# Optimization experiments

Measured on AMD Instinct MI355X. Metric: run time of the kernel, lower is better.

## Reference

```python
import jax, jax.numpy as jnp
import numpy as np

B = 4096          # batch
IN = 4096         # in_features
OUT = 4096        # out_features
MASK_DENSITY = 0.1

def setup_inputs() -> dict:
    key = jax.random.key(0)
    k1, k2, k3, k4, k5 = jax.random.split(key, 5)
    x = jax.random.normal(k1, (B, IN), dtype=jnp.float32)
    # truncated-normal-ish init, std 0.1 (plain normal scaled is fine for a numeric baseline)
    weight = jax.random.normal(k2, (OUT, IN), dtype=jnp.float32) * 0.1
    bound = 1.0 / np.sqrt(IN)
    bias = jax.random.uniform(k3, (OUT,), dtype=jnp.float32, minval=-bound, maxval=bound)
    mask = jax.random.bernoulli(k4, MASK_DENSITY, (OUT, IN))  # bool, fixed sparsity pattern
    residual_connection = jax.random.randint(k5, (OUT,), 0, IN, dtype=jnp.int32)
    return {"x": x, "weight": weight, "bias": bias, "mask": mask,
            "residual_connection": residual_connection}

def reference(x, weight, bias, mask, residual_connection):
    # out = relu(x @ (mask * W)^T + b) + x[:, residual_connection]
    w_masked = jnp.where(mask, weight, 0.0)              # [OUT, IN]
    out = x @ w_masked.T + bias                          # [B, OUT]
    out = jax.nn.relu(out)
    out = jnp.take(x, residual_connection, axis=1) + out # gathered residual add
    return out
```

## Files before the change

kernel.cpp:

```cpp
#include <hip/hip_runtime.h>
#include <hip/hip_bf16.h>
#include <stdint.h>

#define B_ROWS 4096
#define IN_F   4096
#define OUT_F  4096

#define BM 256
#define BN 256
#define BK 64
#define NKT (IN_F / BK)

typedef float  f32x4  __attribute__((ext_vector_type(4)));
typedef short  bf16x8 __attribute__((ext_vector_type(8)));
typedef unsigned short u16x4 __attribute__((ext_vector_type(4)));

#define AS1 __attribute__((address_space(1)))
#define AS3 __attribute__((address_space(3)))

template<int N> struct IC { static constexpr int v = N; };

__device__ __forceinline__ uint16_t f2bf_rne(float f) {
    uint32_t u = __float_as_uint(f);
    uint32_t r = u + 0x7fffu + ((u >> 16) & 1u);
    return (uint16_t)(r >> 16);
}
__device__ __forceinline__ float bf2f(uint16_t h) {
    return __uint_as_float(((uint32_t)h) << 16);
}

__global__ __launch_bounds__(256) void prep_kernel(
    const float* __restrict__ x, uint16_t* __restrict__ xb, uint16_t* __restrict__ xbT,
    const float* __restrict__ w, const void* __restrict__ mraw, uint16_t* __restrict__ wb)
{
    __shared__ float t[64][65];
    __shared__ int flag_s;
    const int tid = threadIdx.x;
    const int blk = blockIdx.x;

    if (blk < 4096) {
        const int r0 = (blk >> 6) * 64;
        const int c0 = (blk & 63) * 64;
        const int lr = tid >> 4;
        const int lc4 = (tid & 15) * 4;

#pragma unroll
        for (int p = 0; p < 4; ++p) {
            const int row = p * 16 + lr;
            float4 v = *(const float4*)(x + (size_t)(r0 + row) * IN_F + c0 + lc4);
            ushort4 o;
            o.x = f2bf_rne(v.x); o.y = f2bf_rne(v.y);
            o.z = f2bf_rne(v.z); o.w = f2bf_rne(v.w);
            *(ushort4*)(xb + (size_t)(r0 + row) * IN_F + c0 + lc4) = o;
            t[row][lc4 + 0] = v.x; t[row][lc4 + 1] = v.y;
            t[row][lc4 + 2] = v.z; t[row][lc4 + 3] = v.w;
        }
        __syncthreads();
#pragma unroll
        for (int p = 0; p < 4; ++p) {
            const int c = p * 16 + lr;
            ushort4 o;
            o.x = f2bf_rne(t[lc4 + 0][c]);
            o.y = f2bf_rne(t[lc4 + 1][c]);
            o.z = f2bf_rne(t[lc4 + 2][c]);
            o.w = f2bf_rne(t[lc4 + 3][c]);
            *(ushort4*)(xbT + (size_t)(c0 + c) * B_ROWS + r0 + lc4) = o;
        }
    } else {
        uint32_t mword = ((const uint32_t*)mraw)[tid];
        unsigned long long bal = __ballot((mword & 0xFFFFFF00u) != 0);
        if (tid == 0) flag_s = 0;
        __syncthreads();
        if (bal != 0ull && (tid & 63) == 0) flag_s = 1;
        __syncthreads();
        const int flag = flag_s;

        const int i = ((blk - 4096) * 256 + tid) * 4;
        float4 v = *(const float4*)(w + i);
        int m0, m1, m2, m3;
        if (flag) {
            uchar4 mm = *(const uchar4*)((const uint8_t*)mraw + i);
            m0 = mm.x; m1 = mm.y; m2 = mm.z; m3 = mm.w;
        } else {
            int4 mm = *(const int4*)((const int*)mraw + i);
            m0 = mm.x; m1 = mm.y; m2 = mm.z; m3 = mm.w;
        }
        ushort4 o;
        o.x = m0 ? f2bf_rne(v.x) : (uint16_t)0;
        o.y = m1 ? f2bf_rne(v.y) : (uint16_t)0;
        o.z = m2 ? f2bf_rne(v.z) : (uint16_t)0;
        o.w = m3 ? f2bf_rne(v.w) : (uint16_t)0;
        *(ushort4*)(wb + i) = o;
    }
}

__device__ __forceinline__ bf16x8 ds_read128(uint32_t off) {
    bf16x8 r;
    asm volatile("ds_read_b128 %0, %1" : "=v"(r) : "v"(off));
    return r;
}
#define LDSOFF(p) ((uint32_t)(uintptr_t)(AS3 void*)(p))

__global__ __launch_bounds__(512, 2) void gemm_kernel(
    const uint16_t* __restrict__ xb, const uint16_t* __restrict__ wb,
    const uint16_t* __restrict__ xbT, const float* __restrict__ bias,
    const int* __restrict__ rc, float* __restrict__ out)
{
    __shared__ alignas(16) uint16_t Abuf[2][2][128 * BK];
    __shared__ alignas(16) uint16_t Bbuf[2][2][128 * BK];
    __shared__ float bias_s[BN];
    __shared__ int   rc_s[BN];

    const int tid = threadIdx.x;

    const int bid = blockIdx.x;
    const int wg  = (bid & 7) * 32 + (bid >> 3);
    const int row0 = (wg >> 4) * BM;
    const int col0 = (wg & 15) * BN;

    const int wave = tid >> 6, lane = tid & 63;
    const int wm = wave >> 2;
    const int wn = wave & 3;
    const int bh = wn >> 1;
    const int quad = lane >> 4, l16 = lane & 15;
    const int swr = (l16 & 7) << 3;
    const int e0  = (quad << 3) ^ swr;
    const uint32_t kd = (uint32_t)(((e0 ^ 32) - e0) * 2);

    const uint32_t aOff0 = LDSOFF(&Abuf[0][wm][0]) + (uint32_t)((l16 * BK + e0) * 2);
    const uint32_t aOff1 = LDSOFF(&Abuf[1][wm][0]) + (uint32_t)((l16 * BK + e0) * 2);
    const uint32_t bOff0 = LDSOFF(&Bbuf[0][bh][0]) + (uint32_t)((((wn & 1) * 64 + l16) * BK + e0) * 2);
    const uint32_t bOff1 = LDSOFF(&Bbuf[1][bh][0]) + (uint32_t)((((wn & 1) * 64 + l16) * BK + e0) * 2);

    const int srow = tid >> 3;
    const int ssw  = ((tid & 7) ^ (srow & 7)) << 3;
    const uint16_t* pA0 = xb + (size_t)(row0 + srow) * IN_F + ssw;
    const uint16_t* pB0 = wb + (size_t)(col0 + srow) * IN_F + ssw;
    const uint16_t* pA1 = pA0 + (size_t)128 * IN_F;
    const uint16_t* pB1 = pB0 + (size_t)128 * IN_F;

    auto stage = [&](const uint16_t* src, uint16_t* ldsdst, size_t ko) {
        __builtin_amdgcn_global_load_lds((const AS1 void*)(src + ko),
                                         (AS3 void*)(ldsdst + tid * 8), 16, 0, 0);
        __builtin_amdgcn_global_load_lds((const AS1 void*)(src + ko + (size_t)64 * IN_F),
                                         (AS3 void*)(ldsdst + tid * 8 + 4096), 16, 0, 0);
    };

    if (tid < BN) {
        __builtin_amdgcn_global_load_lds((const AS1 void*)(bias + col0 + tid),
                                         (AS3 void*)(bias_s + tid), 4, 0, 0);
        __builtin_amdgcn_global_load_lds((const AS1 void*)(rc + col0 + tid),
                                         (AS3 void*)(rc_s + tid), 4, 0, 0);
    }

    f32x4 acc[8][4];
#pragma unroll
    for (int mi = 0; mi < 8; ++mi)
#pragma unroll
        for (int ni = 0; ni < 4; ++ni)
            acc[mi][ni] = (f32x4){0.f, 0.f, 0.f, 0.f};

    stage(pA0, &Abuf[0][0][0], 0);
    stage(pA1, &Abuf[0][1][0], 0);
    stage(pB0, &Bbuf[0][0][0], 0);
    stage(pB1, &Bbuf[0][1][0], 0);

#define LGKM0() do { asm volatile("s_waitcnt lgkmcnt(0)" ::: "memory"); \
                     __builtin_amdgcn_sched_barrier(0); } while (0)

    auto tile = [&](auto curc, int t) {
        constexpr int CUR = decltype(curc)::v;
        constexpr int NXT = CUR ^ 1;
        const uint32_t aB = CUR ? aOff1 : aOff0;
        const uint32_t bB = CUR ? bOff1 : bOff0;
        const size_t koff = (size_t)(t + 1) * BK;

        bf16x8 a[4], b[4];

        asm volatile("s_waitcnt vmcnt(0)" ::: "memory");
        __builtin_amdgcn_s_barrier();
        __builtin_amdgcn_sched_barrier(0);

#pragma unroll
        for (int ni = 0; ni < 4; ++ni) b[ni] = ds_read128(bB + ni * 2048);
#pragma unroll
        for (int m = 0; m < 4; ++m)   a[m]  = ds_read128(aB + m * 2048);
        stage(pA0, &Abuf[NXT][0][0], koff);
        stage(pA1, &Abuf[NXT][1][0], koff);
        LGKM0();
        __builtin_amdgcn_s_setprio(1);
#pragma unroll
        for (int m = 0; m < 4; ++m)
#pragma unroll
            for (int ni = 0; ni < 4; ++ni)
                acc[m][ni] = __builtin_amdgcn_mfma_f32_16x16x32_bf16(a[m], b[ni], acc[m][ni], 0, 0, 0);
        __builtin_amdgcn_s_setprio(0);

#pragma unroll
        for (int m = 0; m < 4; ++m)   a[m] = ds_read128(aB + (4 + m) * 2048);
        stage(pB0, &Bbuf[NXT][0][0], koff);
        stage(pB1, &Bbuf[NXT][1][0], koff);
        LGKM0();
        __builtin_amdgcn_s_setprio(1);
#pragma unroll
        for (int m = 0; m < 4; ++m)
#pragma unroll
            for (int ni = 0; ni < 4; ++ni)
                acc[4 + m][ni] = __builtin_amdgcn_mfma_f32_16x16x32_bf16(a[m], b[ni], acc[4 + m][ni], 0, 0, 0);
        __builtin_amdgcn_s_setprio(0);

#pragma unroll
        for (int ni = 0; ni < 4; ++ni) b[ni] = ds_read128(bB + ni * 2048 + kd);
#pragma unroll
        for (int m = 0; m < 4; ++m)   a[m]  = ds_read128(aB + m * 2048 + kd);
        LGKM0();
        __builtin_amdgcn_s_setprio(1);
#pragma unroll
        for (int m = 0; m < 4; ++m)
#pragma unroll
            for (int ni = 0; ni < 4; ++ni)
                acc[m][ni] = __builtin_amdgcn_mfma_f32_16x16x32_bf16(a[m], b[ni], acc[m][ni], 0, 0, 0);
        __builtin_amdgcn_s_setprio(0);

#pragma unroll
        for (int m = 0; m < 4; ++m)   a[m] = ds_read128(aB + (4 + m) * 2048 + kd);
        LGKM0();
        __builtin_amdgcn_s_setprio(1);
#pragma unroll
        for (int m = 0; m < 4; ++m)
#pragma unroll
            for (int ni = 0; ni < 4; ++ni)
                acc[4 + m][ni] = __builtin_amdgcn_mfma_f32_16x16x32_bf16(a[m], b[ni], acc[4 + m][ni], 0, 0, 0);
        __builtin_amdgcn_s_setprio(0);
    };

    for (int tt = 0; tt < NKT; tt += 2) {
        tile(IC<0>{}, tt);
        tile(IC<1>{}, tt + 1);
    }
#undef LGKM0

#pragma unroll
    for (int ni = 0; ni < 4; ++ni) {
        const int lcol = wn * 64 + ni * 16 + l16;
        const int gcol = col0 + lcol;
        const float bv = bias_s[lcol];
        const int   rv = rc_s[lcol];
#pragma unroll
        for (int mi = 0; mi < 8; ++mi) {
            const int grow0 = row0 + wm * 128 + mi * 16 + quad * 4;
            u16x4 xq = *(const u16x4*)(xbT + (size_t)rv * B_ROWS + grow0);
#pragma unroll
            for (int r = 0; r < 4; ++r) {
                float v = fmaxf(acc[mi][ni][r] + bv, 0.0f) + bf2f(xq[r]);
                out[(size_t)(grow0 + r) * OUT_F + gcol] = v;
            }
        }
    }
}

extern "C" void kernel_launch(void* const* d_in, const int* in_sizes, int n_in,
                              void* d_out, int out_size, void* d_ws, size_t ws_size,
                              hipStream_t stream) {
    const float* x    = (const float*)d_in[0];
    const float* w    = (const float*)d_in[1];
    const float* bias = (const float*)d_in[2];
    const void*  mask = (const void*)d_in[3];
    const int*   rc   = (const int*)d_in[4];
    float* out = (float*)d_out;

    uint16_t* xb   = (uint16_t*)d_ws;
    uint16_t* wb   = xb  + (size_t)B_ROWS * IN_F;
    uint16_t* xbT  = wb  + (size_t)OUT_F * IN_F;

    prep_kernel<<<4096 + 16384, 256, 0, stream>>>(x, xb, xbT, w, mask, wb);

    gemm_kernel<<<dim3((B_ROWS / BM) * (OUT_F / BN)), dim3(512), 0, stream>>>(
        xb, wb, xbT, bias, rc, out);
}
```

Measured before the change: 333.7 us.

## Switch GEMM to 32x32x16 MFMA with partial LDS waits and widen weight prep

```diff
diff --git a/kernel.cpp b/kernel.cpp
--- a/kernel.cpp
+++ b/kernel.cpp
@@ -12,6 +12,7 @@
 #define NKT (IN_F / BK)
 
 typedef float  f32x4  __attribute__((ext_vector_type(4)));
+typedef float  f32x16 __attribute__((ext_vector_type(16)));
 typedef short  bf16x8 __attribute__((ext_vector_type(8)));
 typedef unsigned short u16x4 __attribute__((ext_vector_type(4)));
 
@@ -33,12 +34,11 @@
     const float* __restrict__ x, uint16_t* __restrict__ xb, uint16_t* __restrict__ xbT,
     const float* __restrict__ w, const void* __restrict__ mraw, uint16_t* __restrict__ wb)
 {
-    __shared__ float t[64][65];
-    __shared__ int flag_s;
     const int tid = threadIdx.x;
     const int blk = blockIdx.x;
 
     if (blk < 4096) {
+        __shared__ float t[64][65];
         const int r0 = (blk >> 6) * 64;
         const int c0 = (blk & 63) * 64;
         const int lr = tid >> 4;
@@ -67,30 +67,40 @@
             *(ushort4*)(xbT + (size_t)(c0 + c) * B_ROWS + r0 + lc4) = o;
         }
     } else {
+        __shared__ int wflag[4];
         uint32_t mword = ((const uint32_t*)mraw)[tid];
         unsigned long long bal = __ballot((mword & 0xFFFFFF00u) != 0);
-        if (tid == 0) flag_s = 0;
+        if ((tid & 63) == 0) wflag[tid >> 6] = (bal != 0ull);
         __syncthreads();
-        if (bal != 0ull && (tid & 63) == 0) flag_s = 1;
-        __syncthreads();
-        const int flag = flag_s;
-
-        const int i = ((blk - 4096) * 256 + tid) * 4;
-        float4 v = *(const float4*)(w + i);
-        int m0, m1, m2, m3;
+        const int flag = wflag[0] | wflag[1] | wflag[2] | wflag[3];
+
+        const size_t e = ((size_t)(blk - 4096)) * 2048 + (size_t)tid * 8;
+        float4 v0 = *(const float4*)(w + e);
+        float4 v1 = *(const float4*)(w + e + 4);
+        int m[8];
         if (flag) {
-            uchar4 mm = *(const uchar4*)((const uint8_t*)mraw + i);
-            m0 = mm.x; m1 = mm.y; m2 = mm.z; m3 = mm.w;
+            uint2 mm = *(const uint2*)((const uint8_t*)mraw + e);
+#pragma unroll
+            for (int j = 0; j < 4; ++j) m[j]     = (mm.x >> (8 * j)) & 0xff;
+#pragma unroll
+            for (int j = 0; j < 4; ++j) m[4 + j] = (mm.y >> (8 * j)) & 0xff;
         } else {
-            int4 mm = *(const int4*)((const int*)mraw + i);
-            m0 = mm.x; m1 = mm.y; m2 = mm.z; m3 = mm.w;
+            const int* mp = (const int*)mraw + e;
+            int4 a = *(const int4*)mp;
+            int4 b = *(const int4*)(mp + 4);
+            m[0] = a.x; m[1] = a.y; m[2] = a.z; m[3] = a.w;
+            m[4] = b.x; m[5] = b.y; m[6] = b.z; m[7] = b.w;
         }
-        ushort4 o;
-        o.x = m0 ? f2bf_rne(v.x) : (uint16_t)0;
-        o.y = m1 ? f2bf_rne(v.y) : (uint16_t)0;
-        o.z = m2 ? f2bf_rne(v.z) : (uint16_t)0;
-        o.w = m3 ? f2bf_rne(v.w) : (uint16_t)0;
-        *(ushort4*)(wb + i) = o;
+        bf16x8 o;
+        o[0] = m[0] ? (short)f2bf_rne(v0.x) : (short)0;
+        o[1] = m[1] ? (short)f2bf_rne(v0.y) : (short)0;
+        o[2] = m[2] ? (short)f2bf_rne(v0.z) : (short)0;
+        o[3] = m[3] ? (short)f2bf_rne(v0.w) : (short)0;
+        o[4] = m[4] ? (short)f2bf_rne(v1.x) : (short)0;
+        o[5] = m[5] ? (short)f2bf_rne(v1.y) : (short)0;
+        o[6] = m[6] ? (short)f2bf_rne(v1.z) : (short)0;
+        o[7] = m[7] ? (short)f2bf_rne(v1.w) : (short)0;
+        *(bf16x8*)(wb + e) = o;
     }
 }
 
@@ -122,15 +132,21 @@
     const int wm = wave >> 2;
     const int wn = wave & 3;
     const int bh = wn >> 1;
-    const int quad = lane >> 4, l16 = lane & 15;
-    const int swr = (l16 & 7) << 3;
-    const int e0  = (quad << 3) ^ swr;
-    const uint32_t kd = (uint32_t)(((e0 ^ 32) - e0) * 2);
-
-    const uint32_t aOff0 = LDSOFF(&Abuf[0][wm][0]) + (uint32_t)((l16 * BK + e0) * 2);
-    const uint32_t aOff1 = LDSOFF(&Abuf[1][wm][0]) + (uint32_t)((l16 * BK + e0) * 2);
-    const uint32_t bOff0 = LDSOFF(&Bbuf[0][bh][0]) + (uint32_t)((((wn & 1) * 64 + l16) * BK + e0) * 2);
-    const uint32_t bOff1 = LDSOFF(&Bbuf[1][bh][0]) + (uint32_t)((((wn & 1) * 64 + l16) * BK + e0) * 2);
+    const int l32 = lane & 31;
+    const int hh  = lane >> 5;
+    const int sw  = lane & 7;
+
+    uint32_t kswz[4];
+#pragma unroll
+    for (int kg = 0; kg < 4; ++kg)
+        kswz[kg] = (uint32_t)((((kg << 1) | hh) ^ sw) << 4);
+
+    const uint32_t aRowB = (uint32_t)(l32 * 128);
+    const uint32_t bRowB = (uint32_t)((((wn & 1) * 64) + l32) * 128);
+    const uint32_t aOff0 = LDSOFF(&Abuf[0][wm][0]) + aRowB;
+    const uint32_t aOff1 = LDSOFF(&Abuf[1][wm][0]) + aRowB;
+    const uint32_t bOff0 = LDSOFF(&Bbuf[0][bh][0]) + bRowB;
+    const uint32_t bOff1 = LDSOFF(&Bbuf[1][bh][0]) + bRowB;
 
     const int srow = tid >> 3;
     const int ssw  = ((tid & 7) ^ (srow & 7)) << 3;
@@ -153,19 +169,21 @@
                                          (AS3 void*)(rc_s + tid), 4, 0, 0);
     }
 
-    f32x4 acc[8][4];
-#pragma unroll
-    for (int mi = 0; mi < 8; ++mi)
-#pragma unroll
-        for (int ni = 0; ni < 4; ++ni)
-            acc[mi][ni] = (f32x4){0.f, 0.f, 0.f, 0.f};
+    f32x16 acc[4][2];
+#pragma unroll
+    for (int mt = 0; mt < 4; ++mt)
+#pragma unroll
+        for (int nt = 0; nt < 2; ++nt)
+#pragma unroll
+            for (int r = 0; r < 16; ++r)
+                acc[mt][nt][r] = 0.f;
 
     stage(pA0, &Abuf[0][0][0], 0);
     stage(pA1, &Abuf[0][1][0], 0);
     stage(pB0, &Bbuf[0][0][0], 0);
     stage(pB1, &Bbuf[0][1][0], 0);
 
-#define LGKM0() do { asm volatile("s_waitcnt lgkmcnt(0)" ::: "memory"); \
+#define LGKM(n) do { asm volatile("s_waitcnt lgkmcnt(" #n ")" ::: "memory"); \
                      __builtin_amdgcn_sched_barrier(0); } while (0)
 
     auto tile = [&](auto curc, int t) {
@@ -175,62 +193,64 @@
         const uint32_t bB = CUR ? bOff1 : bOff0;
         const size_t koff = (size_t)(t + 1) * BK;
 
-        bf16x8 a[4], b[4];
+        bf16x8 b[2][4], a0[4], a1[4];
 
         asm volatile("s_waitcnt vmcnt(0)" ::: "memory");
         __builtin_amdgcn_s_barrier();
         __builtin_amdgcn_sched_barrier(0);
 
 #pragma unroll
-        for (int ni = 0; ni < 4; ++ni) b[ni] = ds_read128(bB + ni * 2048);
-#pragma unroll
-        for (int m = 0; m < 4; ++m)   a[m]  = ds_read128(aB + m * 2048);
+        for (int nt = 0; nt < 2; ++nt)
+#pragma unroll
+            for (int kg = 0; kg < 4; ++kg)
+                b[nt][kg] = ds_read128(bB + nt * 4096 + kswz[kg]);
         stage(pA0, &Abuf[NXT][0][0], koff);
         stage(pA1, &Abuf[NXT][1][0], koff);
-        LGKM0();
-        __builtin_amdgcn_s_setprio(1);
-#pragma unroll
-        for (int m = 0; m < 4; ++m)
-#pragma unroll
-            for (int ni = 0; ni < 4; ++ni)
-                acc[m][ni] = __builtin_amdgcn_mfma_f32_16x16x32_bf16(a[m], b[ni], acc[m][ni], 0, 0, 0);
-        __builtin_amdgcn_s_setprio(0);
-
-#pragma unroll
-        for (int m = 0; m < 4; ++m)   a[m] = ds_read128(aB + (4 + m) * 2048);
+#pragma unroll
+        for (int kg = 0; kg < 4; ++kg) a0[kg] = ds_read128(aB + kswz[kg]);
+#pragma unroll
+        for (int kg = 0; kg < 4; ++kg) a1[kg] = ds_read128(aB + 4096 + kswz[kg]);
         stage(pB0, &Bbuf[NXT][0][0], koff);
         stage(pB1, &Bbuf[NXT][1][0], koff);
-        LGKM0();
+
+        LGKM(4);
         __builtin_amdgcn_s_setprio(1);
 #pragma unroll
-        for (int m = 0; m < 4; ++m)
-#pragma unroll
-            for (int ni = 0; ni < 4; ++ni)
-                acc[4 + m][ni] = __builtin_amdgcn_mfma_f32_16x16x32_bf16(a[m], b[ni], acc[4 + m][ni], 0, 0, 0);
+        for (int nt = 0; nt < 2; ++nt)
+#pragma unroll
+            for (int kg = 0; kg < 4; ++kg)
+                acc[0][nt] = __builtin_amdgcn_mfma_f32_32x32x16_bf16(a0[kg], b[nt][kg], acc[0][nt], 0, 0, 0);
         __builtin_amdgcn_s_setprio(0);
-
-#pragma unroll
-        for (int ni = 0; ni < 4; ++ni) b[ni] = ds_read128(bB + ni * 2048 + kd);
-#pragma unroll
-        for (int m = 0; m < 4; ++m)   a[m]  = ds_read128(aB + m * 2048 + kd);
-        LGKM0();
+#pragma unroll
+        for (int kg = 0; kg < 4; ++kg) a0[kg] = ds_read128(aB + 2 * 4096 + kswz[kg]);
+
+        LGKM(4);
         __builtin_amdgcn_s_setprio(1);
 #pragma unroll
-        for (int m = 0; m < 4; ++m)
-#pragma unroll
-            for (int ni = 0; ni < 4; ++ni)
-                acc[m][ni] = __builtin_amdgcn_mfma_f32_16x16x32_bf16(a[m], b[ni], acc[m][ni], 0, 0, 0);
+        for (int nt = 0; nt < 2; ++nt)
+#pragma unroll
+            for (int kg = 0; kg < 4; ++kg)
+                acc[1][nt] = __builtin_amdgcn_mfma_f32_32x32x16_bf16(a1[kg], b[nt][kg], acc[1][nt], 0, 0, 0);
         __builtin_amdgcn_s_setprio(0);
-
-#pragma unroll
-        for (int m = 0; m < 4; ++m)   a[m] = ds_read128(aB + (4 + m) * 2048 + kd);
-        LGKM0();
+#pragma unroll
+        for (int kg = 0; kg < 4; ++kg) a1[kg] = ds_read128(aB + 3 * 4096 + kswz[kg]);
+
+        LGKM(4);
         __builtin_amdgcn_s_setprio(1);
 #pragma unroll
-        for (int m = 0; m < 4; ++m)
-#pragma unroll
-            for (int ni = 0; ni < 4; ++ni)
-                acc[4 + m][ni] = __builtin_amdgcn_mfma_f32_16x16x32_bf16(a[m], b[ni], acc[4 + m][ni], 0, 0, 0);
+        for (int nt = 0; nt < 2; ++nt)
+#pragma unroll
+            for (int kg = 0; kg < 4; ++kg)
+                acc[2][nt] = __builtin_amdgcn_mfma_f32_32x32x16_bf16(a0[kg], b[nt][kg], acc[2][nt], 0, 0, 0);
+        __builtin_amdgcn_s_setprio(0);
+
+        LGKM(0);
+        __builtin_amdgcn_s_setprio(1);
+#pragma unroll
+        for (int nt = 0; nt < 2; ++nt)
+#pragma unroll
+            for (int kg = 0; kg < 4; ++kg)
+                acc[3][nt] = __builtin_amdgcn_mfma_f32_32x32x16_bf16(a1[kg], b[nt][kg], acc[3][nt], 0, 0, 0);
         __builtin_amdgcn_s_setprio(0);
     };
 
@@ -238,22 +258,25 @@
         tile(IC<0>{}, tt);
         tile(IC<1>{}, tt + 1);
     }
-#undef LGKM0
-
-#pragma unroll
-    for (int ni = 0; ni < 4; ++ni) {
-        const int lcol = wn * 64 + ni * 16 + l16;
+#undef LGKM
+
+#pragma unroll
+    for (int nt = 0; nt < 2; ++nt) {
+        const int lcol = wn * 64 + nt * 32 + l32;
         const int gcol = col0 + lcol;
         const float bv = bias_s[lcol];
         const int   rv = rc_s[lcol];
 #pragma unroll
-        for (int mi = 0; mi < 8; ++mi) {
-            const int grow0 = row0 + wm * 128 + mi * 16 + quad * 4;
-            u16x4 xq = *(const u16x4*)(xbT + (size_t)rv * B_ROWS + grow0);
-#pragma unroll
-            for (int r = 0; r < 4; ++r) {
-                float v = fmaxf(acc[mi][ni][r] + bv, 0.0f) + bf2f(xq[r]);
-                out[(size_t)(grow0 + r) * OUT_F + gcol] = v;
+        for (int mt = 0; mt < 4; ++mt) {
+#pragma unroll
+            for (int g = 0; g < 4; ++g) {
+                const int grow0 = row0 + wm * 128 + mt * 32 + g * 8 + hh * 4;
+                u16x4 xq = *(const u16x4*)(xbT + (size_t)rv * B_ROWS + grow0);
+#pragma unroll
+                for (int r = 0; r < 4; ++r) {
+                    float v = fmaxf(acc[mt][nt][g * 4 + r] + bv, 0.0f) + bf2f(xq[r]);
+                    out[(size_t)(grow0 + r) * OUT_F + gcol] = v;
+                }
             }
         }
     }
@@ -273,7 +296,7 @@
     uint16_t* wb   = xb  + (size_t)B_ROWS * IN_F;
     uint16_t* xbT  = wb  + (size_t)OUT_F * IN_F;
 
-    prep_kernel<<<4096 + 16384, 256, 0, stream>>>(x, xb, xbT, w, mask, wb);
+    prep_kernel<<<4096 + 8192, 256, 0, stream>>>(x, xb, xbT, w, mask, wb);
 
     gemm_kernel<<<dim3((B_ROWS / BM) * (OUT_F / BN)), dim3(512), 0, stream>>>(
         xb, wb, xbT, bias, rc, out);
```

After: 345.1 us. +3.4%, slower.

## Prefetch LDS fragments ahead of MFMA groups and widen weight prep per thread

Applied to the files above, without the earlier changes.

```diff
diff --git a/kernel.cpp b/kernel.cpp
--- a/kernel.cpp
+++ b/kernel.cpp
@@ -33,12 +33,11 @@
     const float* __restrict__ x, uint16_t* __restrict__ xb, uint16_t* __restrict__ xbT,
     const float* __restrict__ w, const void* __restrict__ mraw, uint16_t* __restrict__ wb)
 {
-    __shared__ float t[64][65];
-    __shared__ int flag_s;
     const int tid = threadIdx.x;
     const int blk = blockIdx.x;
 
     if (blk < 4096) {
+        __shared__ float t[64][65];
         const int r0 = (blk >> 6) * 64;
         const int c0 = (blk & 63) * 64;
         const int lr = tid >> 4;
@@ -67,30 +66,40 @@
             *(ushort4*)(xbT + (size_t)(c0 + c) * B_ROWS + r0 + lc4) = o;
         }
     } else {
+        __shared__ int wflag[4];
         uint32_t mword = ((const uint32_t*)mraw)[tid];
         unsigned long long bal = __ballot((mword & 0xFFFFFF00u) != 0);
-        if (tid == 0) flag_s = 0;
+        if ((tid & 63) == 0) wflag[tid >> 6] = (bal != 0ull);
         __syncthreads();
-        if (bal != 0ull && (tid & 63) == 0) flag_s = 1;
-        __syncthreads();
-        const int flag = flag_s;
-
-        const int i = ((blk - 4096) * 256 + tid) * 4;
-        float4 v = *(const float4*)(w + i);
-        int m0, m1, m2, m3;
+        const int flag = wflag[0] | wflag[1] | wflag[2] | wflag[3];
+
+        const size_t e = ((size_t)(blk - 4096)) * 2048 + (size_t)tid * 8;
+        float4 v0 = *(const float4*)(w + e);
+        float4 v1 = *(const float4*)(w + e + 4);
+        int m[8];
         if (flag) {
-            uchar4 mm = *(const uchar4*)((const uint8_t*)mraw + i);
-            m0 = mm.x; m1 = mm.y; m2 = mm.z; m3 = mm.w;
+            uint2 mm = *(const uint2*)((const uint8_t*)mraw + e);
+#pragma unroll
+            for (int j = 0; j < 4; ++j) m[j]     = (mm.x >> (8 * j)) & 0xff;
+#pragma unroll
+            for (int j = 0; j < 4; ++j) m[4 + j] = (mm.y >> (8 * j)) & 0xff;
         } else {
-            int4 mm = *(const int4*)((const int*)mraw + i);
-            m0 = mm.x; m1 = mm.y; m2 = mm.z; m3 = mm.w;
-        }
-        ushort4 o;
-        o.x = m0 ? f2bf_rne(v.x) : (uint16_t)0;
-        o.y = m1 ? f2bf_rne(v.y) : (uint16_t)0;
-        o.z = m2 ? f2bf_rne(v.z) : (uint16_t)0;
-        o.w = m3 ? f2bf_rne(v.w) : (uint16_t)0;
-        *(ushort4*)(wb + i) = o;
+            const int* mp = (const int*)mraw + e;
+            int4 a = *(const int4*)mp;
+            int4 b = *(const int4*)(mp + 4);
+            m[0] = a.x; m[1] = a.y; m[2] = a.z; m[3] = a.w;
+            m[4] = b.x; m[5] = b.y; m[6] = b.z; m[7] = b.w;
+        }
+        bf16x8 o;
+        o[0] = m[0] ? (short)f2bf_rne(v0.x) : (short)0;
+        o[1] = m[1] ? (short)f2bf_rne(v0.y) : (short)0;
+        o[2] = m[2] ? (short)f2bf_rne(v0.z) : (short)0;
+        o[3] = m[3] ? (short)f2bf_rne(v0.w) : (short)0;
+        o[4] = m[4] ? (short)f2bf_rne(v1.x) : (short)0;
+        o[5] = m[5] ? (short)f2bf_rne(v1.y) : (short)0;
+        o[6] = m[6] ? (short)f2bf_rne(v1.z) : (short)0;
+        o[7] = m[7] ? (short)f2bf_rne(v1.w) : (short)0;
+        *(bf16x8*)(wb + e) = o;
     }
 }
 
@@ -165,7 +174,7 @@
     stage(pB0, &Bbuf[0][0][0], 0);
     stage(pB1, &Bbuf[0][1][0], 0);
 
-#define LGKM0() do { asm volatile("s_waitcnt lgkmcnt(0)" ::: "memory"); \
+#define LGKM(n) do { asm volatile("s_waitcnt lgkmcnt(" #n ")" ::: "memory"); \
                      __builtin_amdgcn_sched_barrier(0); } while (0)
 
     auto tile = [&](auto curc, int t) {
@@ -175,62 +184,65 @@
         const uint32_t bB = CUR ? bOff1 : bOff0;
         const size_t koff = (size_t)(t + 1) * BK;
 
-        bf16x8 a[4], b[4];
+        bf16x8 b[4], b2[4], a0[4], a1[4], a2[4], a3[4];
 
         asm volatile("s_waitcnt vmcnt(0)" ::: "memory");
         __builtin_amdgcn_s_barrier();
         __builtin_amdgcn_sched_barrier(0);
 
 #pragma unroll
-        for (int ni = 0; ni < 4; ++ni) b[ni] = ds_read128(bB + ni * 2048);
-#pragma unroll
-        for (int m = 0; m < 4; ++m)   a[m]  = ds_read128(aB + m * 2048);
+        for (int ni = 0; ni < 4; ++ni) b[ni]  = ds_read128(bB + ni * 2048);
+#pragma unroll
+        for (int m = 0; m < 4; ++m)    a0[m]  = ds_read128(aB + m * 2048);
+#pragma unroll
+        for (int m = 0; m < 4; ++m)    a1[m]  = ds_read128(aB + (4 + m) * 2048);
         stage(pA0, &Abuf[NXT][0][0], koff);
         stage(pA1, &Abuf[NXT][1][0], koff);
-        LGKM0();
-        __builtin_amdgcn_s_setprio(1);
-#pragma unroll
-        for (int m = 0; m < 4; ++m)
-#pragma unroll
-            for (int ni = 0; ni < 4; ++ni)
-                acc[m][ni] = __builtin_amdgcn_mfma_f32_16x16x32_bf16(a[m], b[ni], acc[m][ni], 0, 0, 0);
-        __builtin_amdgcn_s_setprio(0);
-
-#pragma unroll
-        for (int m = 0; m < 4; ++m)   a[m] = ds_read128(aB + (4 + m) * 2048);
+
+        LGKM(4);
+        __builtin_amdgcn_s_setprio(1);
+#pragma unroll
+        for (int m = 0; m < 4; ++m)
+#pragma unroll
+            for (int ni = 0; ni < 4; ++ni)
+                acc[m][ni] = __builtin_amdgcn_mfma_f32_16x16x32_bf16(a0[m], b[ni], acc[m][ni], 0, 0, 0);
+        __builtin_amdgcn_s_setprio(0);
+
+#pragma unroll
+        for (int m = 0; m < 4; ++m)    a2[m]  = ds_read128(aB + m * 2048 + kd);
         stage(pB0, &Bbuf[NXT][0][0], koff);
         stage(pB1, &Bbuf[NXT][1][0], koff);
-        LGKM0();
-        __builtin_amdgcn_s_setprio(1);
-#pragma unroll
-        for (int m = 0; m < 4; ++m)
-#pragma unroll
-            for (int ni = 0; ni < 4; ++ni)
-                acc[4 + m][ni] = __builtin_amdgcn_mfma_f32_16x16x32_bf16(a[m], b[ni], acc[4 + m][ni], 0, 0, 0);
-        __builtin_amdgcn_s_setprio(0);
-
-#pragma unroll
-        for (int ni = 0; ni < 4; ++ni) b[ni] = ds_read128(bB + ni * 2048 + kd);
-#pragma unroll
-        for (int m = 0; m < 4; ++m)   a[m]  = ds_read128(aB + m * 2048 + kd);
-        LGKM0();
-        __builtin_amdgcn_s_setprio(1);
-#pragma unroll
-        for (int m = 0; m < 4; ++m)
-#pragma unroll
-            for (int ni = 0; ni < 4; ++ni)
-                acc[m][ni] = __builtin_amdgcn_mfma_f32_16x16x32_bf16(a[m], b[ni], acc[m][ni], 0, 0, 0);
-        __builtin_amdgcn_s_setprio(0);
-
-#pragma unroll
-        for (int m = 0; m < 4; ++m)   a[m] = ds_read128(aB + (4 + m) * 2048 + kd);
-        LGKM0();
-        __builtin_amdgcn_s_setprio(1);
-#pragma unroll
-        for (int m = 0; m < 4; ++m)
-#pragma unroll
-            for (int ni = 0; ni < 4; ++ni)
-                acc[4 + m][ni] = __builtin_amdgcn_mfma_f32_16x16x32_bf16(a[m], b[ni], acc[4 + m][ni], 0, 0, 0);
+
+        LGKM(4);
+        __builtin_amdgcn_s_setprio(1);
+#pragma unroll
+        for (int m = 0; m < 4; ++m)
+#pragma unroll
+            for (int ni = 0; ni < 4; ++ni)
+                acc[4 + m][ni] = __builtin_amdgcn_mfma_f32_16x16x32_bf16(a1[m], b[ni], acc[4 + m][ni], 0, 0, 0);
+        __builtin_amdgcn_s_setprio(0);
+
+#pragma unroll
+        for (int ni = 0; ni < 4; ++ni) b2[ni] = ds_read128(bB + ni * 2048 + kd);
+#pragma unroll
+        for (int m = 0; m < 4; ++m)    a3[m]  = ds_read128(aB + (4 + m) * 2048 + kd);
+
+        LGKM(4);
+        __builtin_amdgcn_s_setprio(1);
+#pragma unroll
+        for (int m = 0; m < 4; ++m)
+#pragma unroll
+            for (int ni = 0; ni < 4; ++ni)
+                acc[m][ni] = __builtin_amdgcn_mfma_f32_16x16x32_bf16(a2[m], b2[ni], acc[m][ni], 0, 0, 0);
+        __builtin_amdgcn_s_setprio(0);
+
+        LGKM(0);
+        __builtin_amdgcn_s_setprio(1);
+#pragma unroll
+        for (int m = 0; m < 4; ++m)
+#pragma unroll
+            for (int ni = 0; ni < 4; ++ni)
+                acc[4 + m][ni] = __builtin_amdgcn_mfma_f32_16x16x32_bf16(a3[m], b2[ni], acc[4 + m][ni], 0, 0, 0);
         __builtin_amdgcn_s_setprio(0);
     };
 
@@ -238,7 +250,7 @@
         tile(IC<0>{}, tt);
         tile(IC<1>{}, tt + 1);
     }
-#undef LGKM0
+#undef LGKM
 
 #pragma unroll
     for (int ni = 0; ni < 4; ++ni) {
@@ -273,7 +285,7 @@
     uint16_t* wb   = xb  + (size_t)B_ROWS * IN_F;
     uint16_t* xbT  = wb  + (size_t)OUT_F * IN_F;
 
-    prep_kernel<<<4096 + 16384, 256, 0, stream>>>(x, xb, xbT, w, mask, wb);
+    prep_kernel<<<4096 + 8192, 256, 0, stream>>>(x, xb, xbT, w, mask, wb);
 
     gemm_kernel<<<dim3((B_ROWS / BM) * (OUT_F / BN)), dim3(512), 0, stream>>>(
         xb, wb, xbT, bias, rc, out);
```

Result: no change. 337.2 us (+1.1%).
